# Optimization experiments

Hardware: AMD Instinct MI355X
Metric: run time of the kernel (lower is better)

The kernel has to match this reference:

```python
import jax, jax.numpy as jnp
import numpy as np

B, N, D = 64, 4096, 512
ATT = 128


def setup_inputs() -> dict:
    key = jax.random.key(0)
    ks = jax.random.split(key, 7)
    s = lambda fan_in: 1.0 / np.sqrt(fan_in)
    return {
        "v_I": jax.random.normal(ks[0], (B, N, D), dtype=jnp.float32),
        "v_Q": jax.random.normal(ks[1], (B, D), dtype=jnp.float32),
        "W_I": jax.random.normal(ks[2], (D, ATT), dtype=jnp.float32) * s(D),
        "W_Q": jax.random.normal(ks[3], (D, ATT), dtype=jnp.float32) * s(D),
        "b_Q": jnp.zeros((ATT,), dtype=jnp.float32),
        "W_p": jax.random.normal(ks[4], (ATT, 1), dtype=jnp.float32) * s(ATT),
        "b_p": jnp.zeros((1,), dtype=jnp.float32),
    }


def reference(v_I, v_Q, W_I, W_Q, b_Q, W_p, b_p):
    # v_I: [B, N, D], v_Q: [B, D]
    v_I_att = jnp.tanh(jnp.einsum("bnd,da->bna", v_I, W_I))          # [B, N, A]
    v_Q_att = jnp.tanh(v_Q @ W_Q + b_Q)[:, None, :]                  # [B, 1, A]
    h_A = jnp.tanh(v_I_att + v_Q_att)                                # [B, N, A]
    # dropout is identity in inference/reference mode
    p_I = (jnp.einsum("bna,ao->bno", h_A, W_p) + b_p)[..., 0]        # [B, N]
    p_I_output = jax.nn.softmax(p_I, axis=-1)                        # [B, N]
    v_att = jnp.einsum("bn,bnd->bd", p_I_output, v_I)                # [B, D]
    u = v_att + v_Q                                                  # [B, D]
    return (p_I_output, u)
```

## Files before the change

### kernel.cpp

```cpp
#include <hip/hip_runtime.h>
#include <cstdint>
#include <cstddef>

#define B_ 64
#define N_ 4096
#define D_ 512
#define A_ 128

typedef unsigned short u16;
typedef __attribute__((ext_vector_type(8))) short bf16x8;
typedef __attribute__((ext_vector_type(4))) float f32x4;

__device__ __forceinline__ u16 cvt_bf16(float x) {
    unsigned u = __float_as_uint(x);
    return (u16)((u + 0x7FFFu + ((u >> 16) & 1u)) >> 16);
}
__device__ __forceinline__ unsigned pack2_bf16(float a, float b) {
    unsigned ua = __float_as_uint(a), ub = __float_as_uint(b);
    unsigned ra = (ua + 0x7FFFu + ((ua >> 16) & 1u)) >> 16;
    unsigned rb = (ub + 0x7FFFu + ((ub >> 16) & 1u)) >> 16;
    return ra | (rb << 16);
}
__device__ __forceinline__ float fast_tanh(float x) {
    float ax = fabsf(x);
    float e  = __expf(-2.0f * ax);
    float r  = __fdividef(1.0f - e, 1.0f + e);
    return x < 0.0f ? -r : r;
}

__global__ void k_conv_w(const float* __restrict__ WI, u16* __restrict__ Wbf) {
    int idx = blockIdx.x * 256 + threadIdx.x;
    int a  = idx & 127;
    int d0 = (idx >> 7) << 2;
    ushort4 r;
    r.x = cvt_bf16(WI[(d0 + 0) * A_ + a]);
    r.y = cvt_bf16(WI[(d0 + 1) * A_ + a]);
    r.z = cvt_bf16(WI[(d0 + 2) * A_ + a]);
    r.w = cvt_bf16(WI[(d0 + 3) * A_ + a]);
    *(ushort4*)&Wbf[a * D_ + d0] = r;
}

__global__ void k_qatt(const float* __restrict__ vQ, const float* __restrict__ WQ,
                       const float* __restrict__ bQ, float* __restrict__ qatt) {
    int b = blockIdx.x, a = threadIdx.x;
    __shared__ float sq[D_];
    for (int d = a; d < D_; d += 128) sq[d] = vQ[b * D_ + d];
    __syncthreads();
    float acc = bQ[a];
    #pragma unroll 8
    for (int d = 0; d < D_; ++d) acc += sq[d] * WQ[d * A_ + a];
    qatt[b * A_ + a] = fast_tanh(acc);
}

__global__ void __launch_bounds__(256, 2)
k_gemm(const float* __restrict__ vI, const u16* __restrict__ Wbf,
       const float* __restrict__ qatt, const float* __restrict__ Wp,
       float* __restrict__ p_out) {
    const int b  = blockIdx.y;
    const int n0 = blockIdx.x * 128;
    const int t    = threadIdx.x;
    const int lane = t & 63, wave = t >> 6;
    const int l15  = lane & 15, quad = lane >> 4;

    __shared__ u16 lds_a[128 * 72];
    __shared__ u16 lds_b[128 * 72];

    f32x4 acc[2][8];
    #pragma unroll
    for (int mt = 0; mt < 2; ++mt)
        #pragma unroll
        for (int nt = 0; nt < 8; ++nt)
            acc[mt][nt] = (f32x4){0.f, 0.f, 0.f, 0.f};

    const float* ga = vI + (size_t)(b * N_ + n0) * D_;
    const int srow = t >> 4;
    const int scol = t & 15;

    for (int kr = 0; kr < 8; ++kr) {
        const int k0 = kr * 64;
        #pragma unroll
        for (int s = 0; s < 8; ++s) {
            int row = s * 16 + srow;
            float4 v = *(const float4*)(ga + row * D_ + k0 + scol * 4);
            uint2 w;
            w.x = pack2_bf16(v.x, v.y);
            w.y = pack2_bf16(v.z, v.w);
            *(uint2*)&lds_a[row * 72 + scol * 4] = w;
        }
        #pragma unroll
        for (int s = 0; s < 8; ++s) {
            int row = s * 16 + srow;
            ushort4 w = *(const ushort4*)(Wbf + row * D_ + k0 + scol * 4);
            *(ushort4*)&lds_b[row * 72 + scol * 4] = w;
        }
        __syncthreads();
        #pragma unroll
        for (int ks = 0; ks < 2; ++ks) {
            bf16x8 af[2], bfr[8];
            #pragma unroll
            for (int mt = 0; mt < 2; ++mt)
                af[mt] = *(const bf16x8*)&lds_a[(wave * 32 + mt * 16 + l15) * 72 + ks * 32 + quad * 8];
            #pragma unroll
            for (int nt = 0; nt < 8; ++nt)
                bfr[nt] = *(const bf16x8*)&lds_b[(nt * 16 + l15) * 72 + ks * 32 + quad * 8];
            #pragma unroll
            for (int mt = 0; mt < 2; ++mt)
                #pragma unroll
                for (int nt = 0; nt < 8; ++nt)
                    acc[mt][nt] = __builtin_amdgcn_mfma_f32_16x16x32_bf16(
                        af[mt], bfr[nt], acc[mt][nt], 0, 0, 0);
        }
        __syncthreads();
    }

    float qa_v[8], wp_v[8];
    #pragma unroll
    for (int nt = 0; nt < 8; ++nt) {
        int a = nt * 16 + l15;
        qa_v[nt] = qatt[b * A_ + a];
        wp_v[nt] = Wp[a];
    }
    #pragma unroll
    for (int mt = 0; mt < 2; ++mt) {
        #pragma unroll
        for (int r = 0; r < 4; ++r) {
            float s = 0.f;
            #pragma unroll
            for (int nt = 0; nt < 8; ++nt) {
                float t1 = fast_tanh(acc[mt][nt][r]);
                float h  = fast_tanh(t1 + qa_v[nt]);
                s += h * wp_v[nt];
            }
            s += __shfl_xor(s, 1, 16);
            s += __shfl_xor(s, 2, 16);
            s += __shfl_xor(s, 4, 16);
            s += __shfl_xor(s, 8, 16);
            if (l15 == 0)
                p_out[(size_t)b * N_ + n0 + wave * 32 + mt * 16 + quad * 4 + r] = s;
        }
    }
}

__global__ void k_softmax(float* __restrict__ p, const float* __restrict__ vQ,
                          float* __restrict__ u) {
    int b = blockIdx.x, t = threadIdx.x;
    int lane = t & 63, wave = t >> 6;
    float* pb = p + (size_t)b * N_;
    float v[16];
    #pragma unroll
    for (int i = 0; i < 4; ++i) {
        float4 x = *(const float4*)(pb + i * 1024 + t * 4);
        v[i * 4 + 0] = x.x; v[i * 4 + 1] = x.y; v[i * 4 + 2] = x.z; v[i * 4 + 3] = x.w;
    }
    float m = -1e30f;
    #pragma unroll
    for (int i = 0; i < 16; ++i) m = fmaxf(m, v[i]);
    #pragma unroll
    for (int o = 32; o > 0; o >>= 1) m = fmaxf(m, __shfl_xor(m, o, 64));
    __shared__ float redm[4], reds[4];
    if (lane == 0) redm[wave] = m;
    __syncthreads();
    m = fmaxf(fmaxf(redm[0], redm[1]), fmaxf(redm[2], redm[3]));
    float sum = 0.f;
    #pragma unroll
    for (int i = 0; i < 16; ++i) { v[i] = __expf(v[i] - m); sum += v[i]; }
    #pragma unroll
    for (int o = 32; o > 0; o >>= 1) sum += __shfl_xor(sum, o, 64);
    if (lane == 0) reds[wave] = sum;
    __syncthreads();
    sum = reds[0] + reds[1] + reds[2] + reds[3];
    float inv = 1.0f / sum;
    #pragma unroll
    for (int i = 0; i < 4; ++i) {
        float4 x = { v[i*4+0] * inv, v[i*4+1] * inv, v[i*4+2] * inv, v[i*4+3] * inv };
        *(float4*)(pb + i * 1024 + t * 4) = x;
    }
    u[b * D_ + t]       = vQ[b * D_ + t];
    u[b * D_ + 256 + t] = vQ[b * D_ + 256 + t];
}

__global__ void __launch_bounds__(256)
k_wsum(const float* __restrict__ vI, const float* __restrict__ p,
       float* __restrict__ u) {
    const int b  = blockIdx.y;
    const int n0 = blockIdx.x * 512;
    const int t  = threadIdx.x;
    __shared__ float sp[512];
    sp[t]       = p[(size_t)b * N_ + n0 + t];
    sp[t + 256] = p[(size_t)b * N_ + n0 + 256 + t];
    __syncthreads();
    const int rr = t >> 7;
    const int c  = t & 127;
    const float4* base = (const float4*)(vI + (size_t)(b * N_ + n0 + rr) * D_) + c;
    float a0 = 0.f, a1 = 0.f, a2 = 0.f, a3 = 0.f;
    #pragma unroll 8
    for (int n = 0; n < 512; n += 2) {
        float4 x = base[n * 128];
        float w  = sp[n + rr];
        a0 += w * x.x; a1 += w * x.y; a2 += w * x.z; a3 += w * x.w;
    }
    float* ub = u + b * D_ + c * 4;
    atomicAdd(ub + 0, a0);
    atomicAdd(ub + 1, a1);
    atomicAdd(ub + 2, a2);
    atomicAdd(ub + 3, a3);
}

extern "C" void kernel_launch(void* const* d_in, const int* in_sizes, int n_in,
                              void* d_out, int out_size, void* d_ws, size_t ws_size,
                              hipStream_t stream) {
    const float* vI = (const float*)d_in[0];
    const float* vQ = (const float*)d_in[1];
    const float* WI = (const float*)d_in[2];
    const float* WQ = (const float*)d_in[3];
    const float* bQ = (const float*)d_in[4];
    const float* Wp = (const float*)d_in[5];

    float* out_p = (float*)d_out;
    float* out_u = out_p + (size_t)B_ * N_;

    u16*   Wbf  = (u16*)d_ws;
    float* qatt = (float*)((char*)d_ws + (size_t)A_ * D_ * 2);

    k_conv_w<<<64, 256, 0, stream>>>(WI, Wbf);
    k_qatt<<<B_, 128, 0, stream>>>(vQ, WQ, bQ, qatt);
    k_gemm<<<dim3(N_ / 128, B_), 256, 0, stream>>>(vI, Wbf, qatt, Wp, out_p);
    k_softmax<<<B_, 256, 0, stream>>>(out_p, vQ, out_u);
    k_wsum<<<dim3(N_ / 512, B_), 256, 0, stream>>>(vI, out_p, out_u);
}
```

Baseline: 866.7 us.

## Fuse softmax into GEMM epilogue and wsum, drop LDS staging in GEMM

Merges weight conversion and query attention into one prep kernel, which also initialises u and per-batch sums. The GEMM now loads A and B fragments directly from global memory into registers instead of staging them through LDS. Its epilogue writes unnormalised exp scores and atomically accumulates per-batch sums, and the weighted-sum kernel normalises them and writes the probabilities. This removes the separate softmax kernel and its barriers, but skips max subtraction, so it relies on the scores staying bounded, and the GEMM now reads fragments uncoalesced from global/L2.

```diff
diff --git a/kernel.cpp b/kernel.cpp
--- a/kernel.cpp
+++ b/kernel.cpp
@@ -28,43 +28,49 @@
     return x < 0.0f ? -r : r;
 }
 
-__global__ void k_conv_w(const float* __restrict__ WI, u16* __restrict__ Wbf) {
-    int idx = blockIdx.x * 256 + threadIdx.x;
-    int a  = idx & 127;
-    int d0 = (idx >> 7) << 2;
-    ushort4 r;
-    r.x = cvt_bf16(WI[(d0 + 0) * A_ + a]);
-    r.y = cvt_bf16(WI[(d0 + 1) * A_ + a]);
-    r.z = cvt_bf16(WI[(d0 + 2) * A_ + a]);
-    r.w = cvt_bf16(WI[(d0 + 3) * A_ + a]);
-    *(ushort4*)&Wbf[a * D_ + d0] = r;
-}
-
-__global__ void k_qatt(const float* __restrict__ vQ, const float* __restrict__ WQ,
-                       const float* __restrict__ bQ, float* __restrict__ qatt) {
-    int b = blockIdx.x, a = threadIdx.x;
-    __shared__ float sq[D_];
-    for (int d = a; d < D_; d += 128) sq[d] = vQ[b * D_ + d];
-    __syncthreads();
-    float acc = bQ[a];
-    #pragma unroll 8
-    for (int d = 0; d < D_; ++d) acc += sq[d] * WQ[d * A_ + a];
-    qatt[b * A_ + a] = fast_tanh(acc);
-}
-
-__global__ void __launch_bounds__(256, 2)
+__global__ void k_prep(const float* __restrict__ WI, const float* __restrict__ vQ,
+                       const float* __restrict__ WQ, const float* __restrict__ bQ,
+                       u16* __restrict__ Wbf, float* __restrict__ qatt,
+                       float* __restrict__ sums, float* __restrict__ u) {
+    const int blk = blockIdx.x, t = threadIdx.x;
+    if (blk < 64) {
+        #pragma unroll
+        for (int i = 0; i < 2; ++i) {
+            int item = blk * 256 + i * 128 + t;
+            int a  = item & 127;
+            int d0 = (item >> 7) << 2;
+            ushort4 r;
+            r.x = cvt_bf16(WI[(d0 + 0) * A_ + a]);
+            r.y = cvt_bf16(WI[(d0 + 1) * A_ + a]);
+            r.z = cvt_bf16(WI[(d0 + 2) * A_ + a]);
+            r.w = cvt_bf16(WI[(d0 + 3) * A_ + a]);
+            *(ushort4*)&Wbf[a * D_ + d0] = r;
+        }
+    } else {
+        const int b = blk - 64;
+        __shared__ float sq[D_];
+        for (int d = t; d < D_; d += 128) sq[d] = vQ[b * D_ + d];
+        __syncthreads();
+        float acc = bQ[t];
+        #pragma unroll 8
+        for (int d = 0; d < D_; ++d) acc += sq[d] * WQ[d * A_ + t];
+        qatt[b * A_ + t] = fast_tanh(acc);
+        float4 vq4 = *(const float4*)(vQ + b * D_ + t * 4);
+        *(float4*)(u + b * D_ + t * 4) = vq4;
+        if (t == 0) sums[b] = 0.0f;
+    }
+}
+
+__global__ void __launch_bounds__(256)
 k_gemm(const float* __restrict__ vI, const u16* __restrict__ Wbf,
        const float* __restrict__ qatt, const float* __restrict__ Wp,
-       float* __restrict__ p_out) {
+       float* __restrict__ w_out, float* __restrict__ sums) {
     const int b  = blockIdx.y;
     const int n0 = blockIdx.x * 128;
     const int t    = threadIdx.x;
     const int lane = t & 63, wave = t >> 6;
     const int l15  = lane & 15, quad = lane >> 4;
 
-    __shared__ u16 lds_a[128 * 72];
-    __shared__ u16 lds_b[128 * 72];
-
     f32x4 acc[2][8];
     #pragma unroll
     for (int mt = 0; mt < 2; ++mt)
@@ -72,45 +78,37 @@
         for (int nt = 0; nt < 8; ++nt)
             acc[mt][nt] = (f32x4){0.f, 0.f, 0.f, 0.f};
 
-    const float* ga = vI + (size_t)(b * N_ + n0) * D_;
-    const int srow = t >> 4;
-    const int scol = t & 15;
-
-    for (int kr = 0; kr < 8; ++kr) {
-        const int k0 = kr * 64;
-        #pragma unroll
-        for (int s = 0; s < 8; ++s) {
-            int row = s * 16 + srow;
-            float4 v = *(const float4*)(ga + row * D_ + k0 + scol * 4);
-            uint2 w;
-            w.x = pack2_bf16(v.x, v.y);
-            w.y = pack2_bf16(v.z, v.w);
-            *(uint2*)&lds_a[row * 72 + scol * 4] = w;
-        }
-        #pragma unroll
-        for (int s = 0; s < 8; ++s) {
-            int row = s * 16 + srow;
-            ushort4 w = *(const ushort4*)(Wbf + row * D_ + k0 + scol * 4);
-            *(ushort4*)&lds_b[row * 72 + scol * 4] = w;
-        }
-        __syncthreads();
-        #pragma unroll
-        for (int ks = 0; ks < 2; ++ks) {
-            bf16x8 af[2], bfr[8];
-            #pragma unroll
-            for (int mt = 0; mt < 2; ++mt)
-                af[mt] = *(const bf16x8*)&lds_a[(wave * 32 + mt * 16 + l15) * 72 + ks * 32 + quad * 8];
+    const float* a0p = vI + (size_t)(b * N_ + n0 + wave * 32 + l15) * D_ + quad * 8;
+    const float* a1p = a0p + 16 * D_;
+    const u16* bbase = Wbf + (size_t)l15 * D_ + quad * 8;
+
+    #pragma unroll 2
+    for (int kk = 0; kk < 16; ++kk) {
+        const int ko = kk * 32;
+        float4 a0a = *(const float4*)(a0p + ko);
+        float4 a0b = *(const float4*)(a0p + ko + 4);
+        float4 a1a = *(const float4*)(a1p + ko);
+        float4 a1b = *(const float4*)(a1p + ko + 4);
+        bf16x8 bfr[8];
+        #pragma unroll
+        for (int nt = 0; nt < 8; ++nt)
+            bfr[nt] = *(const bf16x8*)(bbase + nt * 16 * D_ + ko);
+        union { bf16x8 v; unsigned u[4]; } c0, c1;
+        c0.u[0] = pack2_bf16(a0a.x, a0a.y);
+        c0.u[1] = pack2_bf16(a0a.z, a0a.w);
+        c0.u[2] = pack2_bf16(a0b.x, a0b.y);
+        c0.u[3] = pack2_bf16(a0b.z, a0b.w);
+        c1.u[0] = pack2_bf16(a1a.x, a1a.y);
+        c1.u[1] = pack2_bf16(a1a.z, a1a.w);
+        c1.u[2] = pack2_bf16(a1b.x, a1b.y);
+        c1.u[3] = pack2_bf16(a1b.z, a1b.w);
+        bf16x8 af[2] = { c0.v, c1.v };
+        #pragma unroll
+        for (int mt = 0; mt < 2; ++mt)
             #pragma unroll
             for (int nt = 0; nt < 8; ++nt)
-                bfr[nt] = *(const bf16x8*)&lds_b[(nt * 16 + l15) * 72 + ks * 32 + quad * 8];
-            #pragma unroll
-            for (int mt = 0; mt < 2; ++mt)
-                #pragma unroll
-                for (int nt = 0; nt < 8; ++nt)
-                    acc[mt][nt] = __builtin_amdgcn_mfma_f32_16x16x32_bf16(
-                        af[mt], bfr[nt], acc[mt][nt], 0, 0, 0);
-        }
-        __syncthreads();
+                acc[mt][nt] = __builtin_amdgcn_mfma_f32_16x16x32_bf16(
+                    af[mt], bfr[nt], acc[mt][nt], 0, 0, 0);
     }
 
     float qa_v[8], wp_v[8];
@@ -120,6 +118,7 @@
         qa_v[nt] = qatt[b * A_ + a];
         wp_v[nt] = Wp[a];
     }
+    float lsum = 0.f;
     #pragma unroll
     for (int mt = 0; mt < 2; ++mt) {
         #pragma unroll
@@ -135,69 +134,42 @@
             s += __shfl_xor(s, 2, 16);
             s += __shfl_xor(s, 4, 16);
             s += __shfl_xor(s, 8, 16);
+            float we = __expf(s);
+            lsum += we;
             if (l15 == 0)
-                p_out[(size_t)b * N_ + n0 + wave * 32 + mt * 16 + quad * 4 + r] = s;
+                w_out[(size_t)b * N_ + n0 + wave * 32 + mt * 16 + quad * 4 + r] = we;
         }
     }
-}
-
-__global__ void k_softmax(float* __restrict__ p, const float* __restrict__ vQ,
-                          float* __restrict__ u) {
-    int b = blockIdx.x, t = threadIdx.x;
-    int lane = t & 63, wave = t >> 6;
-    float* pb = p + (size_t)b * N_;
-    float v[16];
-    #pragma unroll
-    for (int i = 0; i < 4; ++i) {
-        float4 x = *(const float4*)(pb + i * 1024 + t * 4);
-        v[i * 4 + 0] = x.x; v[i * 4 + 1] = x.y; v[i * 4 + 2] = x.z; v[i * 4 + 3] = x.w;
-    }
-    float m = -1e30f;
-    #pragma unroll
-    for (int i = 0; i < 16; ++i) m = fmaxf(m, v[i]);
-    #pragma unroll
-    for (int o = 32; o > 0; o >>= 1) m = fmaxf(m, __shfl_xor(m, o, 64));
-    __shared__ float redm[4], reds[4];
-    if (lane == 0) redm[wave] = m;
+    lsum += __shfl_xor(lsum, 16, 64);
+    lsum += __shfl_xor(lsum, 32, 64);
+    __shared__ float wred[4];
+    if (lane == 0) wred[wave] = lsum;
     __syncthreads();
-    m = fmaxf(fmaxf(redm[0], redm[1]), fmaxf(redm[2], redm[3]));
-    float sum = 0.f;
-    #pragma unroll
-    for (int i = 0; i < 16; ++i) { v[i] = __expf(v[i] - m); sum += v[i]; }
-    #pragma unroll
-    for (int o = 32; o > 0; o >>= 1) sum += __shfl_xor(sum, o, 64);
-    if (lane == 0) reds[wave] = sum;
-    __syncthreads();
-    sum = reds[0] + reds[1] + reds[2] + reds[3];
-    float inv = 1.0f / sum;
-    #pragma unroll
-    for (int i = 0; i < 4; ++i) {
-        float4 x = { v[i*4+0] * inv, v[i*4+1] * inv, v[i*4+2] * inv, v[i*4+3] * inv };
-        *(float4*)(pb + i * 1024 + t * 4) = x;
-    }
-    u[b * D_ + t]       = vQ[b * D_ + t];
-    u[b * D_ + 256 + t] = vQ[b * D_ + 256 + t];
+    if (t == 0) atomicAdd(sums + b, wred[0] + wred[1] + wred[2] + wred[3]);
 }
 
 __global__ void __launch_bounds__(256)
-k_wsum(const float* __restrict__ vI, const float* __restrict__ p,
+k_wsum(const float* __restrict__ vI, const float* __restrict__ w,
+       const float* __restrict__ sums, float* __restrict__ p_out,
        float* __restrict__ u) {
     const int b  = blockIdx.y;
-    const int n0 = blockIdx.x * 512;
+    const int n0 = blockIdx.x * 256;
     const int t  = threadIdx.x;
-    __shared__ float sp[512];
-    sp[t]       = p[(size_t)b * N_ + n0 + t];
-    sp[t + 256] = p[(size_t)b * N_ + n0 + 256 + t];
+    const float inv = 1.0f / sums[b];
+    __shared__ float sp[256];
+    float pv = w[(size_t)b * N_ + n0 + t] * inv;
+    sp[t] = pv;
+    p_out[(size_t)b * N_ + n0 + t] = pv;
     __syncthreads();
     const int rr = t >> 7;
     const int c  = t & 127;
     const float4* base = (const float4*)(vI + (size_t)(b * N_ + n0 + rr) * D_) + c;
     float a0 = 0.f, a1 = 0.f, a2 = 0.f, a3 = 0.f;
     #pragma unroll 8
-    for (int n = 0; n < 512; n += 2) {
+    for (int n = 0; n < 256; n += 2) {
         float4 x = base[n * 128];
-        float w  = sp[n + rr];
-        a0 += w * x.x; a1 += w * x.y; a2 += w * x.z; a3 += w * x.w;
+        float wn = sp[n + rr];
+        a0 += wn * x.x; a1 += wn * x.y; a2 += wn * x.z; a3 += wn * x.w;
     }
     float* ub = u + b * D_ + c * 4;
     atomicAdd(ub + 0, a0);
@@ -219,12 +191,13 @@
     float* out_p = (float*)d_out;
     float* out_u = out_p + (size_t)B_ * N_;
 
-    u16*   Wbf  = (u16*)d_ws;
-    float* qatt = (float*)((char*)d_ws + (size_t)A_ * D_ * 2);
-
-    k_conv_w<<<64, 256, 0, stream>>>(WI, Wbf);
-    k_qatt<<<B_, 128, 0, stream>>>(vQ, WQ, bQ, qatt);
-    k_gemm<<<dim3(N_ / 128, B_), 256, 0, stream>>>(vI, Wbf, qatt, Wp, out_p);
-    k_softmax<<<B_, 256, 0, stream>>>(out_p, vQ, out_u);
-    k_wsum<<<dim3(N_ / 512, B_), 256, 0, stream>>>(vI, out_p, out_u);
-}
+    char* ws = (char*)d_ws;
+    u16*   Wbf  = (u16*)ws;
+    float* qatt = (float*)(ws + 131072);
+    float* sums = (float*)(ws + 131072 + 32768);
+    float* wbuf = (float*)(ws + 131072 + 32768 + 1024);
+
+    k_prep<<<128, 128, 0, stream>>>(WI, vQ, WQ, bQ, Wbf, qatt, sums, out_u);
+    k_gemm<<<dim3(N_ / 128, B_), 256, 0, stream>>>(vI, Wbf, qatt, Wp, wbuf, sums);
+    k_wsum<<<dim3(N_ / 256, B_), 256, 0, stream>>>(vI, wbuf, sums, out_p, out_u);
+}
```

After: 873.2 us. Within noise of the previous version (+0.8%).
